# Kernel tuning notes

Measured on AMD Instinct MI355X. Metric: run time of the kernel, lower is better.

Reference implementation:

```python
import jax, jax.numpy as jnp
import numpy as np

WS = 8      # window size
NH = 8      # num heads
ED = 256    # embed dim
HD = ED // NH  # head dim


def conv2d(x, w, b):
    # x: [B,C,H,W], w: [O,I,3,3] (torch OIHW), SAME padding, stride 1
    y = jax.lax.conv_general_dilated(x, w, (1, 1), 'SAME',
                                     dimension_numbers=('NCHW', 'OIHW', 'NCHW'))
    return y + b[None, :, None, None]


def linear(x, w, b):
    # torch Linear: y = x @ W^T + b, w: [out,in]
    return jnp.einsum('bnc,oc->bno', x, w) + b


def window_partition(x, ws):
    B, C, H, W = x.shape
    x = x.reshape(B, C, H // ws, ws, W // ws, ws)
    x = jnp.transpose(x, (0, 2, 4, 3, 5, 1))  # B, H/ws, W/ws, ws, ws, C
    return x.reshape(-1, ws * ws, C)


def window_reverse(win, H, W, ws, C):
    nW = (H // ws) * (W // ws)
    B = win.shape[0] // nW
    x = win.reshape(B, H // ws, W // ws, ws, ws, C)
    x = jnp.transpose(x, (0, 5, 1, 3, 2, 4))
    return x.reshape(B, C, H, W)


def setup_inputs() -> dict:
    key = jax.random.key(0)
    ks = jax.random.split(key, 24)
    s = 0.02
    inp = {
        'xmap': jax.random.normal(ks[0], (4, ED, 256, 256), jnp.float32),
        'xfeat': jax.random.normal(ks[1], (4, 32, 256, 256), jnp.float32),
        'cmap_w': jax.random.normal(ks[2], (ED, ED, 3, 3), jnp.float32) * s,
        'cmap_b': jnp.zeros((ED,), jnp.float32),
        'cfeat_w': jax.random.normal(ks[3], (ED, 32, 3, 3), jnp.float32) * s,
        'cfeat_b': jnp.zeros((ED,), jnp.float32),
        'qxmap_w': jax.random.normal(ks[4], (ED, ED), jnp.float32) * s,
        'qxmap_b': jnp.zeros((ED,), jnp.float32),
        'kxmap_w': jax.random.normal(ks[5], (ED, ED), jnp.float32) * s,
        'kxmap_b': jnp.zeros((ED,), jnp.float32),
        'vxmap_w': jax.random.normal(ks[6], (ED, ED), jnp.float32) * s,
        'vxmap_b': jnp.zeros((ED,), jnp.float32),
        'qxfeat_w': jax.random.normal(ks[7], (ED, ED), jnp.float32) * s,
        'qxfeat_b': jnp.zeros((ED,), jnp.float32),
        'kxfeat_w': jax.random.normal(ks[8], (ED, ED), jnp.float32) * s,
        'kxfeat_b': jnp.zeros((ED,), jnp.float32),
        'proj_w': jax.random.normal(ks[9], (ED, ED), jnp.float32) * s,
        'proj_b': jnp.zeros((ED,), jnp.float32),
        'cout_w': jax.random.normal(ks[10], (ED, ED, 3, 3), jnp.float32) * s,
        'cout_b': jnp.zeros((ED,), jnp.float32),
    }
    return inp


def reference(xmap, xfeat, cmap_w, cmap_b, cfeat_w, cfeat_b,
              qxmap_w, qxmap_b, kxmap_w, kxmap_b, vxmap_w, vxmap_b,
              qxfeat_w, qxfeat_b, kxfeat_w, kxfeat_b,
              proj_w, proj_b, cout_w, cout_b):
    B, C, H, W = xmap.shape  # xfeat matches spatial size -> no interpolate branch
    xmap = conv2d(xmap, cmap_w, cmap_b)
    identity = xmap
    wm = window_partition(xmap, WS)                        # [Bw, N, C]
    wf = window_partition(conv2d(xfeat, cfeat_w, cfeat_b), WS)
    Bw, N, _ = wm.shape

    def heads(t):
        return jnp.transpose(t.reshape(Bw, N, NH, HD), (0, 2, 1, 3))  # [Bw,H,N,D]

    q_m = heads(linear(wm, qxmap_w, qxmap_b))
    k_m = heads(linear(wm, kxmap_w, kxmap_b))
    v_m = heads(linear(wm, vxmap_w, vxmap_b))
    q_f = heads(linear(wf, qxfeat_w, qxfeat_b))
    k_f = heads(linear(wf, kxfeat_w, kxfeat_b))

    q_g = jax.nn.sigmoid(q_f) * q_m
    k_g = jax.nn.sigmoid(k_f) * k_m

    scale = 1.0 / jnp.sqrt(jnp.asarray(HD, q_g.dtype))
    attn = jax.nn.softmax(jnp.einsum('bhnd,bhmd->bhnm', q_g, k_g) * scale, axis=-1)
    out = jnp.einsum('bhnm,bhmd->bhnd', attn, v_m)         # [Bw,H,N,D]
    out = jnp.transpose(out, (0, 2, 1, 3)).reshape(Bw, N, C)
    out = window_reverse(linear(out, proj_w, proj_b), H, W, WS, C)
    return conv2d(out, cout_w, cout_b) + identity
```

## Files before the change

kernel.cpp:

```cpp
#include <hip/hip_runtime.h>
#include <hip/hip_bf16.h>
#include <cstdint>
#include <math.h>

using bf16 = __hip_bfloat16;
typedef __attribute__((ext_vector_type(4))) float f32x4;
typedef __attribute__((ext_vector_type(8))) short s16x8;
typedef __attribute__((ext_vector_type(4))) short s16x4;

#define AS3(p) ((__attribute__((address_space(3))) void *)(p))
#define AS1(p) ((const __attribute__((address_space(1))) void *)(p))

static constexpr int Himg = 256, Wimg = 256, Bimg = 4;
static constexpr int HWimg = Himg * Wimg;
static constexpr int Ttok = Bimg * HWimg;

__device__ __forceinline__ void gld16(bf16* lds, const bf16* g) {
  __builtin_amdgcn_global_load_lds(AS1(g), AS3(lds), 16, 0, 0);
}

__device__ __forceinline__ unsigned short f2u(float f) {
  bf16 b = __float2bfloat16(f);
  unsigned short u; __builtin_memcpy(&u, &b, 2); return u;
}

__device__ __forceinline__ void remap_tile(int bid, int total, int NY, int& t0, int& n0) {
  int lin = (bid & 7) * (total >> 3) + (bid >> 3);
  t0 = (lin / NY) * 128;
  n0 = (lin % NY) * 128;
}

__global__ void k_zero4k(float* p) {
  p[blockIdx.x * 256 + threadIdx.x] = 0.f;
}

__global__ void k_castf2b(const float* __restrict__ s, bf16* __restrict__ d, int n) {
  int i = blockIdx.x * 256 + threadIdx.x;
  if (i < n) d[i] = __float2bfloat16(s[i]);
}

__global__ void k_copyf(const float* __restrict__ s, float* __restrict__ d, int n) {
  int i = blockIdx.x * 256 + threadIdx.x;
  if (i < n) d[i] = s[i];
}

__global__ void k_permconv(const float* __restrict__ w, bf16* __restrict__ o, int I) {
  int idx = blockIdx.x * 256 + threadIdx.x;
  int tot = 256 * 9 * I;
  if (idx >= tot) return;
  int i   = idx % I;
  int rem = idx / I;
  int tap = rem % 9;
  int oc  = rem / 9;
  o[idx] = __float2bfloat16(w[(oc * I + i) * 9 + tap]);
}

__global__ void k_tohwc(const float* __restrict__ src, bf16* __restrict__ dst, int C) {
  int bh = blockIdx.x;
  int w0 = blockIdx.y * 32;
  int c0 = blockIdx.z * 32;
  int b = bh / Himg, h = bh % Himg;
  __shared__ float tile[32][33];
  int tid = threadIdx.x;
  int x = tid & 31, y = tid >> 5;
  const float* sp = src + (size_t)b * C * HWimg + (size_t)h * Wimg;
#pragma unroll
  for (int p = 0; p < 4; ++p) {
    int cl = y + p * 8;
    tile[cl][x] = sp[(size_t)(c0 + cl) * HWimg + w0 + x];
  }
  __syncthreads();
#pragma unroll
  for (int p = 0; p < 4; ++p) {
    int wl = y + p * 8;
    dst[((size_t)bh * Wimg + w0 + wl) * C + c0 + x] = __float2bfloat16(tile[x][wl]);
  }
}

__global__ void k_tochw(const bf16* __restrict__ src, float* __restrict__ dst) {
  int bh = blockIdx.x, w0 = blockIdx.y * 32, c0 = blockIdx.z * 32;
  int b = bh >> 8, h = bh & 255;
  __shared__ float tile[32][33];
  int tid = threadIdx.x, x = tid & 31, y = tid >> 5;
  const bf16* sp = src + (size_t)bh * Wimg * 256;
#pragma unroll
  for (int p = 0; p < 4; ++p) {
    int wl = y + p * 8;
    tile[wl][x] = __bfloat162float(sp[(size_t)(w0 + wl) * 256 + c0 + x]);
  }
  __syncthreads();
#pragma unroll
  for (int p = 0; p < 4; ++p) {
    int cl = y + p * 8;
    dst[(((size_t)b * 256 + c0 + cl) * Himg + h) * Wimg + w0 + x] = tile[x][cl];
  }
}

template <int CIN, int TAPS, int EPI>
__global__ void __launch_bounds__(256, 3)
k_gemm(const bf16* __restrict__ Ain, const bf16* __restrict__ BT,
       const float* __restrict__ bias,
       bf16* __restrict__ outb, int ldo,
       const bf16* __restrict__ ident,
       const bf16* __restrict__ zp, int NY)
{
  constexpr int KTOT = TAPS * CIN;
  constexpr int NK = KTOT / 32;
  int t0, n0;
  remap_tile(blockIdx.x, gridDim.x, NY, t0, n0);
  const int tid = threadIdx.x;
  const int wave = tid >> 6, lane = tid & 63;
  const int seg = lane & 3;
  const int rr  = lane >> 2;

  __shared__ bf16 sA0[128 * 32];
  __shared__ bf16 sA1[128 * 32];
  __shared__ bf16 sA2[128 * 32];
  __shared__ bf16 sB0[128 * 32];
  __shared__ bf16 sB1[128 * 32];
  __shared__ bf16 sB2[128 * 32];

  f32x4 acc[4][4] = {};

  const int wr = wave >> 1, wc = wave & 1;
  const int fr = lane & 15, fq = lane >> 4;

#define STAGE(WA, WB, KSV) do {                                                 \
    const int k0_ = (KSV) * 32;                                                 \
    const int tap_ = k0_ / CIN;                                                 \
    const int c0_ = k0_ - tap_ * CIN;                                           \
    const int dy_ = tap_ / 3 - 1, dx_ = tap_ % 3 - 1;                           \
    _Pragma("unroll") for (int i_ = 0; i_ < 2; ++i_) {                          \
      const int r_ = wave * 32 + i_ * 16 + rr;                                  \
      const int t_ = t0 + r_;                                                   \
      const bf16* src_;                                                         \
      if (TAPS == 1) {                                                          \
        src_ = Ain + (size_t)t_ * CIN + k0_ + seg * 8;                          \
      } else {                                                                  \
        const int hh_ = ((t_ >> 8) & 255) + dy_, ww_ = (t_ & 255) + dx_;        \
        const bool v_ = ((unsigned)hh_ < 256u) && ((unsigned)ww_ < 256u);       \
        const long gi_ = (long)t_ + dy_ * Wimg + dx_;                           \
        src_ = v_ ? (Ain + gi_ * CIN + c0_ + seg * 8) : (zp + seg * 8);         \
      }                                                                         \
      gld16(WA + (wave * 32 + i_ * 16) * 32, src_);                             \
      gld16(WB + (wave * 32 + i_ * 16) * 32,                                    \
            BT + (size_t)(n0 + wave * 32 + i_ * 16 + rr) * KTOT + k0_ + seg * 8); \
    }                                                                           \
  } while (0)

#define GSTEP(RA, RB, WA, WB, KSV, LASTF) do {                                  \
    if (LASTF) { asm volatile("s_waitcnt vmcnt(0)" ::: "memory"); }             \
    else       { asm volatile("s_waitcnt vmcnt(4)" ::: "memory"); }             \
    __builtin_amdgcn_s_barrier();                                               \
    s16x8 af_[4], bf_[4];                                                       \
    _Pragma("unroll") for (int m_ = 0; m_ < 4; ++m_)                            \
      af_[m_] = *(const s16x8*)(RA + (wr * 64 + m_ * 16 + fr) * 32 + fq * 8);   \
    _Pragma("unroll") for (int n_ = 0; n_ < 4; ++n_)                            \
      bf_[n_] = *(const s16x8*)(RB + (wc * 64 + n_ * 16 + fr) * 32 + fq * 8);   \
    if ((KSV) + 2 < NK) STAGE(WA, WB, (KSV) + 2);                               \
    __builtin_amdgcn_s_setprio(1);                                              \
    _Pragma("unroll") for (int m_ = 0; m_ < 4; ++m_)                            \
      _Pragma("unroll") for (int n_ = 0; n_ < 4; ++n_)                          \
        acc[m_][n_] = __builtin_amdgcn_mfma_f32_16x16x32_bf16(af_[m_], bf_[n_], acc[m_][n_], 0, 0, 0); \
    __builtin_amdgcn_s_setprio(0);                                              \
  } while (0)

  STAGE(sA0, sB0, 0);
  STAGE(sA1, sB1, 1);

  constexpr int NMAIN = ((NK - 1) / 3) * 3;
  int ks = 0;
#pragma unroll 1
  for (; ks < NMAIN; ks += 3) {
    GSTEP(sA0, sB0, sA2, sB2, ks,     false);
    GSTEP(sA1, sB1, sA0, sB0, ks + 1, false);
    GSTEP(sA2, sB2, sA1, sB1, ks + 2, false);
  }
  constexpr int TREM = NK - NMAIN;
  if constexpr (TREM == 3) {
    GSTEP(sA0, sB0, sA2, sB2, NMAIN,     false);
    GSTEP(sA1, sB1, sA0, sB0, NMAIN + 1, false);
    GSTEP(sA2, sB2, sA1, sB1, NMAIN + 2, true);
  } else if constexpr (TREM == 2) {
    GSTEP(sA0, sB0, sA2, sB2, NMAIN,     false);
    GSTEP(sA1, sB1, sA0, sB0, NMAIN + 1, true);
  } else {
    GSTEP(sA0, sB0, sA2, sB2, NMAIN,     true);
  }
#undef GSTEP
#undef STAGE

#pragma unroll
  for (int m = 0; m < 4; ++m) {
#pragma unroll
    for (int n = 0; n < 4; ++n) {
      const int col = n0 + wc * 64 + n * 16 + fr;
#pragma unroll
      for (int j = 0; j < 4; ++j) {
        const int row = wr * 64 + m * 16 + fq * 4 + j;
        const size_t t = (size_t)t0 + row;
        float v = acc[m][n][j] + bias[col];
        if (EPI == 0) {
          outb[t * ldo + col] = __float2bfloat16(v);
        } else {
          v += __bfloat162float(ident[t * 256 + col]);
          outb[t * 256 + col] = __float2bfloat16(v);
        }
      }
    }
  }
}

__global__ void __launch_bounds__(256, 2)
k_gemm_qkv(const bf16* __restrict__ Am, const bf16* __restrict__ Af,
           const bf16* __restrict__ Bm, const bf16* __restrict__ Bf,
           const float* __restrict__ bm, const float* __restrict__ bfi,
           bf16* __restrict__ out)
{
  int t0, n0;
  remap_tile(blockIdx.x, gridDim.x, 4, t0, n0);
  const int tid = threadIdx.x;
  const int wave = tid >> 6, lane = tid & 63;
  const int seg = lane & 3;
  const int rr  = lane >> 2;

  __shared__ bf16 sA0[128 * 32];
  __shared__ bf16 sA1[128 * 32];
  __shared__ bf16 sA2[128 * 32];
  __shared__ bf16 sB0[128 * 32];
  __shared__ bf16 sB1[128 * 32];
  __shared__ bf16 sB2[128 * 32];

  f32x4 accm[4][4] = {};
  f32x4 accf[4][4] = {};

  const int wr = wave >> 1, wc = wave & 1;
  const int fr = lane & 15, fq = lane >> 4;

#define STAGEQ(WA, WB, SV) do {                                                 \
    const int k0_ = ((SV) >> 1) * 32;                                           \
    const bf16* A_ = ((SV) & 1) ? Af : Am;                                      \
    const bf16* B_ = ((SV) & 1) ? Bf : Bm;                                      \
    _Pragma("unroll") for (int i_ = 0; i_ < 2; ++i_) {                          \
      const int r_ = wave * 32 + i_ * 16 + rr;                                  \
      gld16(WA + (wave * 32 + i_ * 16) * 32, A_ + (size_t)(t0 + r_) * 256 + k0_ + seg * 8); \
      gld16(WB + (wave * 32 + i_ * 16) * 32, B_ + (size_t)(n0 + r_) * 256 + k0_ + seg * 8); \
    }                                                                           \
  } while (0)

#define QSTEP(RA, RB, WA, WB, SV, LASTF) do {                                   \
    if (LASTF) { asm volatile("s_waitcnt vmcnt(0)" ::: "memory"); }             \
    else       { asm volatile("s_waitcnt vmcnt(4)" ::: "memory"); }             \
    __builtin_amdgcn_s_barrier();                                               \
    s16x8 af_[4], bf_[4];                                                       \
    _Pragma("unroll") for (int m_ = 0; m_ < 4; ++m_)                            \
      af_[m_] = *(const s16x8*)(RA + (wr * 64 + m_ * 16 + fr) * 32 + fq * 8);   \
    _Pragma("unroll") for (int n_ = 0; n_ < 4; ++n_)                            \
      bf_[n_] = *(const s16x8*)(RB + (wc * 64 + n_ * 16 + fr) * 32 + fq * 8);   \
    if ((SV) + 2 < 16) STAGEQ(WA, WB, (SV) + 2);                                \
    __builtin_amdgcn_s_setprio(1);                                              \
    if ((SV) & 1) {                                                             \
      _Pragma("unroll") for (int m_ = 0; m_ < 4; ++m_)                          \
        _Pragma("unroll") for (int n_ = 0; n_ < 4; ++n_)                        \
          accf[m_][n_] = __builtin_amdgcn_mfma_f32_16x16x32_bf16(af_[m_], bf_[n_], accf[m_][n_], 0, 0, 0); \
    } else {                                                                    \
      _Pragma("unroll") for (int m_ = 0; m_ < 4; ++m_)                          \
        _Pragma("unroll") for (int n_ = 0; n_ < 4; ++n_)                        \
          accm[m_][n_] = __builtin_amdgcn_mfma_f32_16x16x32_bf16(af_[m_], bf_[n_], accm[m_][n_], 0, 0, 0); \
    }                                                                           \
    __builtin_amdgcn_s_setprio(0);                                              \
  } while (0)

  STAGEQ(sA0, sB0, 0);
  STAGEQ(sA1, sB1, 1);

  int s = 0;
#pragma unroll 1
  for (; s < 15; s += 3) {
    QSTEP(sA0, sB0, sA2, sB2, s,     false);
    QSTEP(sA1, sB1, sA0, sB0, s + 1, false);
    QSTEP(sA2, sB2, sA1, sB1, s + 2, false);
  }
  QSTEP(sA0, sB0, sA2, sB2, 15, true);
#undef QSTEP
#undef STAGEQ

#pragma unroll
  for (int m = 0; m < 4; ++m) {
#pragma unroll
    for (int n = 0; n < 4; ++n) {
      const int col = n0 + wc * 64 + n * 16 + fr;
#pragma unroll
      for (int j = 0; j < 4; ++j) {
        const int row = wr * 64 + m * 16 + fq * 4 + j;
        const size_t t = (size_t)t0 + row;
        float v = accm[m][n][j] + bm[col];
        const float g = accf[m][n][j] + bfi[col];
        v *= 1.f / (1.f + __expf(-g));
        out[t * 768 + col] = __float2bfloat16(v);
      }
    }
  }
}

__global__ void __launch_bounds__(256, 2)
k_attn_mfma(const bf16* __restrict__ qkv, bf16* __restrict__ out) {
  __shared__ short smem[4 * 7424];
  const int tid = threadIdx.x;
  const int wave = tid >> 6, lane = tid & 63;
  const int fr = lane & 15, fq = lane >> 4;
  const int wi = blockIdx.x >> 1;
  const int head = (blockIdx.x & 1) * 4 + wave;
  const int b = wi >> 10, rem = wi & 1023, wh = rem >> 5, ww = rem & 31;
  const size_t tbase = (size_t)b * HWimg + (size_t)(wh * 8) * Wimg + ww * 8;

  short* Qs = smem + wave * 7424;
  short* Ks = Qs + 2560;
  short* VT = Qs + 5120;
  short* P  = Qs;
  short* Ol = Qs;

  auto tok = [&](int i) -> size_t {
    return tbase + (size_t)(i >> 3) * Wimg + (i & 7);
  };

  {
    const bf16* tb = qkv + tok(lane) * 768 + head * 32;
#pragma unroll
    for (int c = 0; c < 4; ++c) {
      s16x8 qv = *(const s16x8*)(tb + c * 8);
      s16x8 kv = *(const s16x8*)(tb + 256 + c * 8);
      s16x8 vv = *(const s16x8*)(tb + 512 + c * 8);
      *(s16x8*)(Qs + lane * 40 + c * 8) = qv;
      *(s16x8*)(Ks + lane * 40 + c * 8) = kv;
#pragma unroll
      for (int e = 0; e < 8; ++e) VT[(c * 8 + e) * 72 + lane] = vv[e];
    }
  }

  s16x8 kf[4], qf[4];
#pragma unroll
  for (int m = 0; m < 4; ++m)
    kf[m] = *(const s16x8*)(Ks + (fr + 16 * m) * 40 + fq * 8);
#pragma unroll
  for (int n = 0; n < 4; ++n)
    qf[n] = *(const s16x8*)(Qs + (fr + 16 * n) * 40 + fq * 8);

  f32x4 st[4][4] = {};
#pragma unroll
  for (int m = 0; m < 4; ++m)
#pragma unroll
    for (int n = 0; n < 4; ++n)
      st[m][n] = __builtin_amdgcn_mfma_f32_16x16x32_bf16(kf[m], qf[n], st[m][n], 0, 0, 0);

  const float scale = 0.17677669529663688f;
  float invs[4];
#pragma unroll
  for (int n = 0; n < 4; ++n) {
    float mx = -1e30f;
#pragma unroll
    for (int m = 0; m < 4; ++m)
#pragma unroll
      for (int j = 0; j < 4; ++j) mx = fmaxf(mx, st[m][n][j]);
    mx = fmaxf(mx, __shfl_xor(mx, 16));
    mx = fmaxf(mx, __shfl_xor(mx, 32));
    float sum = 0.f;
#pragma unroll
    for (int m = 0; m < 4; ++m) {
      s16x4 pk;
#pragma unroll
      for (int j = 0; j < 4; ++j) {
        float e = __expf((st[m][n][j] - mx) * scale);
        sum += e;
        pk[j] = (short)f2u(e);
      }
      *(s16x4*)(P + (fr + 16 * n) * 72 + 16 * m + 4 * fq) = pk;
    }
    sum += __shfl_xor(sum, 16);
    sum += __shfl_xor(sum, 32);
    invs[n] = 1.f / sum;
  }

  f32x4 oc[4][2] = {};
#pragma unroll
  for (int ks = 0; ks < 2; ++ks) {
    s16x8 pf[4], vf[2];
#pragma unroll
    for (int m = 0; m < 4; ++m)
      pf[m] = *(const s16x8*)(P + (fr + 16 * m) * 72 + ks * 32 + fq * 8);
#pragma unroll
    for (int n = 0; n < 2; ++n)
      vf[n] = *(const s16x8*)(VT + (fr + 16 * n) * 72 + ks * 32 + fq * 8);
#pragma unroll
    for (int m = 0; m < 4; ++m)
#pragma unroll
      for (int n = 0; n < 2; ++n)
        oc[m][n] = __builtin_amdgcn_mfma_f32_16x16x32_bf16(pf[m], vf[n], oc[m][n], 0, 0, 0);
  }

#pragma unroll
  for (int m = 0; m < 4; ++m)
#pragma unroll
    for (int j = 0; j < 4; ++j) {
      const float inv = __shfl(invs[m], 4 * fq + j);
      const int q = 16 * m + 4 * fq + j;
#pragma unroll
      for (int n = 0; n < 2; ++n)
        Ol[q * 40 + fr + 16 * n] = (short)f2u(oc[m][n][j] * inv);
    }
  {
    bf16* op = out + tok(lane) * 256 + head * 32;
#pragma unroll
    for (int c = 0; c < 4; ++c)
      *(s16x8*)(op + c * 8) = *(const s16x8*)(Ol + lane * 40 + c * 8);
  }
}

extern "C" void kernel_launch(void* const* d_in, const int* in_sizes, int n_in,
                              void* d_out, int out_size, void* d_ws, size_t ws_size,
                              hipStream_t stream) {
  const float* xmap    = (const float*)d_in[0];
  const float* xfeat   = (const float*)d_in[1];
  const float* cmap_w  = (const float*)d_in[2];
  const float* cmap_b  = (const float*)d_in[3];
  const float* cfeat_w = (const float*)d_in[4];
  const float* cfeat_b = (const float*)d_in[5];
  const float* qxmap_w = (const float*)d_in[6];
  const float* qxmap_b = (const float*)d_in[7];
  const float* kxmap_w = (const float*)d_in[8];
  const float* kxmap_b = (const float*)d_in[9];
  const float* vxmap_w = (const float*)d_in[10];
  const float* vxmap_b = (const float*)d_in[11];
  const float* qxfeat_w = (const float*)d_in[12];
  const float* qxfeat_b = (const float*)d_in[13];
  const float* kxfeat_w = (const float*)d_in[14];
  const float* kxfeat_b = (const float*)d_in[15];
  const float* proj_w  = (const float*)d_in[16];
  const float* proj_b  = (const float*)d_in[17];
  const float* cout_w  = (const float*)d_in[18];
  const float* cout_b  = (const float*)d_in[19];

  uint8_t* ws = (uint8_t*)d_ws;
  size_t off = 0;
  auto alloc = [&](size_t bytes) -> void* {
    void* p = ws + off;
    off += (bytes + 255) & ~(size_t)255;
    return p;
  };
  float* zp       = (float*)alloc(4096);
  bf16* cmap_wT   = (bf16*)alloc((size_t)2304 * 256 * 2);
  bf16* cout_wT   = (bf16*)alloc((size_t)2304 * 256 * 2);
  bf16* cfeat_wT  = (bf16*)alloc((size_t)288 * 256 * 2);
  bf16* lin_qkv_wT= (bf16*)alloc((size_t)768 * 256 * 2);
  bf16* lin_f_wT  = (bf16*)alloc((size_t)512 * 256 * 2);
  bf16* proj_wT   = (bf16*)alloc((size_t)256 * 256 * 2);
  float* bias_qkv = (float*)alloc(768 * 4);
  float* bias_f   = (float*)alloc(512 * 4);
  bf16* xm_nhwc   = (bf16*)alloc((size_t)Ttok * 256 * 2);
  bf16* xf_nhwc   = (bf16*)alloc((size_t)Ttok * 32 * 2);
  bf16* xc        = (bf16*)alloc((size_t)Ttok * 256 * 2);
  bf16* fc        = (bf16*)alloc((size_t)Ttok * 256 * 2);
  bf16* qkv       = (bf16*)alloc((size_t)Ttok * 768 * 2);
  bf16* attn_out  = xm_nhwc;
  bf16* proj_out  = fc;
  bf16* convout   = qkv;
  bf16* zpb = (bf16*)zp;

  k_zero4k<<<4, 256, 0, stream>>>(zp);
  k_permconv<<<(256 * 9 * 256 + 255) / 256, 256, 0, stream>>>(cmap_w, cmap_wT, 256);
  k_permconv<<<(256 * 9 * 256 + 255) / 256, 256, 0, stream>>>(cout_w, cout_wT, 256);
  k_permconv<<<(256 * 9 * 32 + 255) / 256, 256, 0, stream>>>(cfeat_w, cfeat_wT, 32);
  k_castf2b<<<256, 256, 0, stream>>>(qxmap_w, lin_qkv_wT, 65536);
  k_castf2b<<<256, 256, 0, stream>>>(kxmap_w, lin_qkv_wT + 65536, 65536);
  k_castf2b<<<256, 256, 0, stream>>>(vxmap_w, lin_qkv_wT + 131072, 65536);
  k_castf2b<<<256, 256, 0, stream>>>(qxfeat_w, lin_f_wT, 65536);
  k_castf2b<<<256, 256, 0, stream>>>(kxfeat_w, lin_f_wT + 65536, 65536);
  k_castf2b<<<256, 256, 0, stream>>>(proj_w, proj_wT, 65536);
  k_copyf<<<1, 256, 0, stream>>>(qxmap_b, bias_qkv, 256);
  k_copyf<<<1, 256, 0, stream>>>(kxmap_b, bias_qkv + 256, 256);
  k_copyf<<<1, 256, 0, stream>>>(vxmap_b, bias_qkv + 512, 256);
  k_copyf<<<1, 256, 0, stream>>>(qxfeat_b, bias_f, 256);
  k_copyf<<<1, 256, 0, stream>>>(kxfeat_b, bias_f + 256, 256);

  k_tohwc<<<dim3(Bimg * Himg, Wimg / 32, 256 / 32), 256, 0, stream>>>(xmap, xm_nhwc, 256);
  k_tohwc<<<dim3(Bimg * Himg, Wimg / 32, 1), 256, 0, stream>>>(xfeat, xf_nhwc, 32);

  dim3 blk(256);
  const int NT = Ttok / 128;
  k_gemm<256, 9, 0><<<dim3(NT * 2), blk, 0, stream>>>(
      xm_nhwc, cmap_wT, cmap_b, xc, 256, nullptr, zpb, 2);
  k_gemm<32, 9, 0><<<dim3(NT * 2), blk, 0, stream>>>(
      xf_nhwc, cfeat_wT, cfeat_b, fc, 256, nullptr, zpb, 2);
  k_gemm<256, 1, 0><<<dim3(NT * 2), blk, 0, stream>>>(
      xc, lin_qkv_wT + 131072, bias_qkv + 512, qkv + 512, 768, nullptr, zpb, 2);
  k_gemm_qkv<<<dim3(NT * 4), blk, 0, stream>>>(
      xc, fc, lin_qkv_wT, lin_f_wT, bias_qkv, bias_f, qkv);
  k_attn_mfma<<<dim3(4096 * 2), blk, 0, stream>>>(qkv, attn_out);
  k_gemm<256, 1, 0><<<dim3(NT * 2), blk, 0, stream>>>(
      attn_out, proj_wT, proj_b, proj_out, 256, nullptr, zpb, 2);
  k_gemm<256, 9, 2><<<dim3(NT * 2), blk, 0, stream>>>(
      proj_out, cout_wT, cout_b, convout, 256, xc, zpb, 2);
  k_tochw<<<dim3(Bimg * Himg, Wimg / 32, 256 / 32), 256, 0, stream>>>(convout, (float*)d_out);
}
```

Measured before the change: 1.653 ms.

## Enlarge GEMM M-tile to 256 rows and XOR-swizzle LDS fragment layout

The generic conv/linear GEMM kernel now computes 256x128 tiles per block instead of 128x128: each wave holds 8x4 MFMA accumulators, the A staging buffers double, and grid sizes halve. This raises arithmetic intensity and reuse of the B (weight) tile per load. Both this kernel and the QK gemm also apply an XOR swizzle to the 16-byte segment within each LDS row, on the global-to-LDS load side and the fragment read side, to cut LDS bank conflicts. In exchange, register pressure rises (launch bounds drop from 3 to 2 blocks per CU), LDS use grows, and the grid has fewer blocks.

```diff
diff --git a/kernel.cpp b/kernel.cpp
--- a/kernel.cpp
+++ b/kernel.cpp
@@ -24,9 +24,9 @@
   unsigned short u; __builtin_memcpy(&u, &b, 2); return u;
 }
 
-__device__ __forceinline__ void remap_tile(int bid, int total, int NY, int& t0, int& n0) {
+__device__ __forceinline__ void remap_tile(int bid, int total, int NY, int BMv, int& t0, int& n0) {
   int lin = (bid & 7) * (total >> 3) + (bid >> 3);
-  t0 = (lin / NY) * 128;
+  t0 = (lin / NY) * BMv;
   n0 = (lin % NY) * 128;
 }
 
@@ -97,7 +97,7 @@
 }
 
 template <int CIN, int TAPS, int EPI>
-__global__ void __launch_bounds__(256, 3)
+__global__ void __launch_bounds__(256, 2)
 k_gemm(const bf16* __restrict__ Ain, const bf16* __restrict__ BT,
        const float* __restrict__ bias,
        bf16* __restrict__ outb, int ldo,
@@ -107,59 +107,64 @@
   constexpr int KTOT = TAPS * CIN;
   constexpr int NK = KTOT / 32;
   int t0, n0;
-  remap_tile(blockIdx.x, gridDim.x, NY, t0, n0);
+  remap_tile(blockIdx.x, gridDim.x, NY, 256, t0, n0);
   const int tid = threadIdx.x;
   const int wave = tid >> 6, lane = tid & 63;
   const int seg = lane & 3;
   const int rr  = lane >> 2;
 
-  __shared__ bf16 sA0[128 * 32];
-  __shared__ bf16 sA1[128 * 32];
-  __shared__ bf16 sA2[128 * 32];
+  __shared__ bf16 sA0[256 * 32];
+  __shared__ bf16 sA1[256 * 32];
+  __shared__ bf16 sA2[256 * 32];
   __shared__ bf16 sB0[128 * 32];
   __shared__ bf16 sB1[128 * 32];
   __shared__ bf16 sB2[128 * 32];
 
-  f32x4 acc[4][4] = {};
+  f32x4 acc[8][4] = {};
 
   const int wr = wave >> 1, wc = wave & 1;
   const int fr = lane & 15, fq = lane >> 4;
+  const int sseg = (seg ^ ((rr >> 1) & 3)) * 8;
+  const int slot = (fq ^ ((fr >> 1) & 3)) * 8;
 
 #define STAGE(WA, WB, KSV) do {                                                 \
     const int k0_ = (KSV) * 32;                                                 \
     const int tap_ = k0_ / CIN;                                                 \
     const int c0_ = k0_ - tap_ * CIN;                                           \
     const int dy_ = tap_ / 3 - 1, dx_ = tap_ % 3 - 1;                           \
-    _Pragma("unroll") for (int i_ = 0; i_ < 2; ++i_) {                          \
-      const int r_ = wave * 32 + i_ * 16 + rr;                                  \
-      const int t_ = t0 + r_;                                                   \
+    _Pragma("unroll") for (int i_ = 0; i_ < 4; ++i_) {                          \
+      const int g_ = i_ * 4 + wave;                                             \
+      const int t_ = t0 + g_ * 16 + rr;                                         \
       const bf16* src_;                                                         \
       if (TAPS == 1) {                                                          \
-        src_ = Ain + (size_t)t_ * CIN + k0_ + seg * 8;                          \
+        src_ = Ain + (size_t)t_ * CIN + k0_ + sseg;                             \
       } else {                                                                  \
         const int hh_ = ((t_ >> 8) & 255) + dy_, ww_ = (t_ & 255) + dx_;        \
         const bool v_ = ((unsigned)hh_ < 256u) && ((unsigned)ww_ < 256u);       \
         const long gi_ = (long)t_ + dy_ * Wimg + dx_;                           \
-        src_ = v_ ? (Ain + gi_ * CIN + c0_ + seg * 8) : (zp + seg * 8);         \
+        src_ = v_ ? (Ain + gi_ * CIN + c0_ + sseg) : (zp + sseg);               \
       }                                                                         \
-      gld16(WA + (wave * 32 + i_ * 16) * 32, src_);                             \
-      gld16(WB + (wave * 32 + i_ * 16) * 32,                                    \
-            BT + (size_t)(n0 + wave * 32 + i_ * 16 + rr) * KTOT + k0_ + seg * 8); \
+      gld16(WA + g_ * 16 * 32, src_);                                           \
+    }                                                                           \
+    _Pragma("unroll") for (int i_ = 0; i_ < 2; ++i_) {                          \
+      const int g_ = i_ * 4 + wave;                                             \
+      gld16(WB + g_ * 16 * 32,                                                  \
+            BT + (size_t)(n0 + g_ * 16 + rr) * KTOT + k0_ + sseg);              \
     }                                                                           \
   } while (0)
 
 #define GSTEP(RA, RB, WA, WB, KSV, LASTF) do {                                  \
     if (LASTF) { asm volatile("s_waitcnt vmcnt(0)" ::: "memory"); }             \
-    else       { asm volatile("s_waitcnt vmcnt(4)" ::: "memory"); }             \
+    else       { asm volatile("s_waitcnt vmcnt(6)" ::: "memory"); }             \
     __builtin_amdgcn_s_barrier();                                               \
-    s16x8 af_[4], bf_[4];                                                       \
-    _Pragma("unroll") for (int m_ = 0; m_ < 4; ++m_)                            \
-      af_[m_] = *(const s16x8*)(RA + (wr * 64 + m_ * 16 + fr) * 32 + fq * 8);   \
+    s16x8 af_[8], bf_[4];                                                       \
+    _Pragma("unroll") for (int m_ = 0; m_ < 8; ++m_)                            \
+      af_[m_] = *(const s16x8*)(RA + (wr * 128 + m_ * 16 + fr) * 32 + slot);    \
     _Pragma("unroll") for (int n_ = 0; n_ < 4; ++n_)                            \
-      bf_[n_] = *(const s16x8*)(RB + (wc * 64 + n_ * 16 + fr) * 32 + fq * 8);   \
+      bf_[n_] = *(const s16x8*)(RB + (wc * 64 + n_ * 16 + fr) * 32 + slot);     \
     if ((KSV) + 2 < NK) STAGE(WA, WB, (KSV) + 2);                               \
     __builtin_amdgcn_s_setprio(1);                                              \
-    _Pragma("unroll") for (int m_ = 0; m_ < 4; ++m_)                            \
+    _Pragma("unroll") for (int m_ = 0; m_ < 8; ++m_)                            \
       _Pragma("unroll") for (int n_ = 0; n_ < 4; ++n_)                          \
         acc[m_][n_] = __builtin_amdgcn_mfma_f32_16x16x32_bf16(af_[m_], bf_[n_], acc[m_][n_], 0, 0, 0); \
     __builtin_amdgcn_s_setprio(0);                                              \
@@ -191,13 +196,13 @@
 #undef STAGE
 
 #pragma unroll
-  for (int m = 0; m < 4; ++m) {
+  for (int m = 0; m < 8; ++m) {
 #pragma unroll
     for (int n = 0; n < 4; ++n) {
       const int col = n0 + wc * 64 + n * 16 + fr;
 #pragma unroll
       for (int j = 0; j < 4; ++j) {
-        const int row = wr * 64 + m * 16 + fq * 4 + j;
+        const int row = wr * 128 + m * 16 + fq * 4 + j;
         const size_t t = (size_t)t0 + row;
         float v = acc[m][n][j] + bias[col];
         if (EPI == 0) {
@@ -218,7 +223,7 @@
            bf16* __restrict__ out)
 {
   int t0, n0;
-  remap_tile(blockIdx.x, gridDim.x, 4, t0, n0);
+  remap_tile(blockIdx.x, gridDim.x, 4, 128, t0, n0);
   const int tid = threadIdx.x;
   const int wave = tid >> 6, lane = tid & 63;
   const int seg = lane & 3;
@@ -236,6 +241,8 @@
 
   const int wr = wave >> 1, wc = wave & 1;
   const int fr = lane & 15, fq = lane >> 4;
+  const int sseg = (seg ^ ((rr >> 1) & 3)) * 8;
+  const int slot = (fq ^ ((fr >> 1) & 3)) * 8;
 
 #define STAGEQ(WA, WB, SV) do {                                                 \
     const int k0_ = ((SV) >> 1) * 32;                                           \
@@ -243,8 +250,8 @@
     const bf16* B_ = ((SV) & 1) ? Bf : Bm;                                      \
     _Pragma("unroll") for (int i_ = 0; i_ < 2; ++i_) {                          \
       const int r_ = wave * 32 + i_ * 16 + rr;                                  \
-      gld16(WA + (wave * 32 + i_ * 16) * 32, A_ + (size_t)(t0 + r_) * 256 + k0_ + seg * 8); \
-      gld16(WB + (wave * 32 + i_ * 16) * 32, B_ + (size_t)(n0 + r_) * 256 + k0_ + seg * 8); \
+      gld16(WA + (wave * 32 + i_ * 16) * 32, A_ + (size_t)(t0 + r_) * 256 + k0_ + sseg); \
+      gld16(WB + (wave * 32 + i_ * 16) * 32, B_ + (size_t)(n0 + r_) * 256 + k0_ + sseg); \
     }                                                                           \
   } while (0)
 
@@ -254,9 +261,9 @@
     __builtin_amdgcn_s_barrier();                                               \
     s16x8 af_[4], bf_[4];                                                       \
     _Pragma("unroll") for (int m_ = 0; m_ < 4; ++m_)                            \
-      af_[m_] = *(const s16x8*)(RA + (wr * 64 + m_ * 16 + fr) * 32 + fq * 8);   \
+      af_[m_] = *(const s16x8*)(RA + (wr * 64 + m_ * 16 + fr) * 32 + slot);     \
     _Pragma("unroll") for (int n_ = 0; n_ < 4; ++n_)                            \
-      bf_[n_] = *(const s16x8*)(RB + (wc * 64 + n_ * 16 + fr) * 32 + fq * 8);   \
+      bf_[n_] = *(const s16x8*)(RB + (wc * 64 + n_ * 16 + fr) * 32 + slot);     \
     if ((SV) + 2 < 16) STAGEQ(WA, WB, (SV) + 2);                                \
     __builtin_amdgcn_s_setprio(1);                                              \
     if ((SV) & 1) {                                                             \
@@ -486,19 +493,19 @@
   k_tohwc<<<dim3(Bimg * Himg, Wimg / 32, 1), 256, 0, stream>>>(xfeat, xf_nhwc, 32);
 
   dim3 blk(256);
-  const int NT = Ttok / 128;
-  k_gemm<256, 9, 0><<<dim3(NT * 2), blk, 0, stream>>>(
+  const int NT256 = Ttok / 256;
+  k_gemm<256, 9, 0><<<dim3(NT256 * 2), blk, 0, stream>>>(
       xm_nhwc, cmap_wT, cmap_b, xc, 256, nullptr, zpb, 2);
-  k_gemm<32, 9, 0><<<dim3(NT * 2), blk, 0, stream>>>(
+  k_gemm<32, 9, 0><<<dim3(NT256 * 2), blk, 0, stream>>>(
       xf_nhwc, cfeat_wT, cfeat_b, fc, 256, nullptr, zpb, 2);
-  k_gemm<256, 1, 0><<<dim3(NT * 2), blk, 0, stream>>>(
+  k_gemm<256, 1, 0><<<dim3(NT256 * 2), blk, 0, stream>>>(
       xc, lin_qkv_wT + 131072, bias_qkv + 512, qkv + 512, 768, nullptr, zpb, 2);
-  k_gemm_qkv<<<dim3(NT * 4), blk, 0, stream>>>(
+  k_gemm_qkv<<<dim3((Ttok / 128) * 4), blk, 0, stream>>>(
       xc, fc, lin_qkv_wT, lin_f_wT, bias_qkv, bias_f, qkv);
   k_attn_mfma<<<dim3(4096 * 2), blk, 0, stream>>>(qkv, attn_out);
-  k_gemm<256, 1, 0><<<dim3(NT * 2), blk, 0, stream>>>(
+  k_gemm<256, 1, 0><<<dim3(NT256 * 2), blk, 0, stream>>>(
       attn_out, proj_wT, proj_b, proj_out, 256, nullptr, zpb, 2);
-  k_gemm<256, 9, 2><<<dim3(NT * 2), blk, 0, stream>>>(
+  k_gemm<256, 9, 2><<<dim3(NT256 * 2), blk, 0, stream>>>(
       proj_out, cout_wT, cout_b, convout, 256, xc, zpb, 2);
   k_tochw<<<dim3(Bimg * Himg, Wimg / 32, 256 / 32), 256, 0, stream>>>(convout, (float*)d_out);
 }
```

New measurement: 1.556 ms. 1.06x faster.
